# Kernel optimization log

Hardware: AMD Instinct MI355X
Metric: run time of the kernel (lower is better)

Reference implementation:

```python
import jax, jax.numpy as jnp
import numpy as np

N = 6144
INPUT_SIZE = 1024
HIDDEN = 256
NEG_INF = -9e15  # matches torch masked_fill value -9000000000000000.0


def setup_inputs() -> dict:
    key = jax.random.key(0)
    k1, k2, k3, k4 = jax.random.split(key, 4)
    nodes_embed = jax.random.normal(k1, (N, INPUT_SIZE), dtype=jnp.float32)
    node_adj = jax.random.randint(k2, (N, N), 0, 2, dtype=jnp.int32)
    # learned params (xavier-uniform-ish scaling)
    limW = np.sqrt(6.0 / (INPUT_SIZE + HIDDEN))
    W = jax.random.uniform(k3, (INPUT_SIZE, HIDDEN), minval=-limW, maxval=limW, dtype=jnp.float32)
    lima = 1.414 * np.sqrt(6.0 / (2 * HIDDEN + 1))
    a_edge = jax.random.uniform(k4, (2 * HIDDEN,), minval=-lima, maxval=lima, dtype=jnp.float32)
    return {"nodes_embed": nodes_embed, "W": W, "a_edge": a_edge, "node_adj": node_adj}


def reference(nodes_embed, W, a_edge, node_adj):
    # h = nodes_embed @ W : [N, hidden]
    h = nodes_embed @ W
    # W_edge([h_i ; h_j]) decomposes exactly: (h_i @ a1) + (h_j @ a2)
    a1, a2 = a_edge[:HIDDEN], a_edge[HIDDEN:]
    score = (h @ a1)[:, None] + (h @ a2)[None, :]  # [N, N]
    adj_f = node_adj.astype(h.dtype)
    weight = jax.nn.leaky_relu(adj_f * score, negative_slope=0.2)
    weight = jnp.where(node_adj == 0, jnp.asarray(NEG_INF, h.dtype), weight)
    attention = jax.nn.softmax(weight, axis=-1)
    # dropout in eval mode (identity)
    return attention @ h  # [N, hidden]
```

## Files before the change

### kernel.cpp

```cpp
#include <hip/hip_runtime.h>
#include <hip/hip_bf16.h>

#define NN 6144
#define INPUT 1024
#define HID 256

using frag  = __attribute__((ext_vector_type(8))) short;
using f32x4 = __attribute__((ext_vector_type(4))) float;

static __device__ __forceinline__ unsigned short bf16u(float x) {
    unsigned u = __float_as_uint(x);
    u += 0x7fff + ((u >> 16) & 1);
    return (unsigned short)(u >> 16);
}

__global__ __launch_bounds__(256) void k_convert_w(const float* __restrict__ W,
                                                   unsigned short* __restrict__ Wt) {
    int t = blockIdx.x * 256 + threadIdx.x;
    int n = t >> 10, k = t & 1023;
    Wt[t] = bf16u(W[k * HID + n]);
}

__global__ __launch_bounds__(256) void k_gemm1(const float* __restrict__ X,
                                               const unsigned short* __restrict__ Wt,
                                               const float* __restrict__ a_edge,
                                               unsigned short* __restrict__ hT,
                                               float* __restrict__ s1,
                                               float* __restrict__ s2) {
    __shared__ unsigned short A[2][32][72];
    int t = threadIdx.x;
    int m = t >> 3, cg = t & 7;
    int i0 = blockIdx.x * 32, n0 = blockIdx.y * 64;
    int w = t >> 6, l = t & 63, lm = l & 15, q = l >> 4;
    int nw = n0 + w * 16;

    const float* xrow = X + (size_t)(i0 + m) * INPUT + cg * 8;
    const unsigned short* brow = Wt + (size_t)(nw + lm) * INPUT + q * 8;

    f32x4 acc0 = {}, acc1 = {};

    for (int c = 0; c < 16; c++) {
        int buf = c & 1;
        float4 xa = *reinterpret_cast<const float4*>(xrow + c * 64);
        float4 xb = *reinterpret_cast<const float4*>(xrow + c * 64 + 4);
        frag av;
        av[0] = (short)bf16u(xa.x); av[1] = (short)bf16u(xa.y);
        av[2] = (short)bf16u(xa.z); av[3] = (short)bf16u(xa.w);
        av[4] = (short)bf16u(xb.x); av[5] = (short)bf16u(xb.y);
        av[6] = (short)bf16u(xb.z); av[7] = (short)bf16u(xb.w);
        *reinterpret_cast<frag*>(&A[buf][m][cg * 8]) = av;

        __syncthreads();

#pragma unroll
        for (int kk = 0; kk < 2; kk++) {
            frag a0 = *reinterpret_cast<const frag*>(&A[buf][lm][kk * 32 + q * 8]);
            frag a1 = *reinterpret_cast<const frag*>(&A[buf][16 + lm][kk * 32 + q * 8]);
            frag b  = *reinterpret_cast<const frag*>(brow + c * 64 + kk * 32);
            acc0 = __builtin_amdgcn_mfma_f32_16x16x32_bf16(a0, b, acc0, 0, 0, 0);
            acc1 = __builtin_amdgcn_mfma_f32_16x16x32_bf16(a1, b, acc1, 0, 0, 0);
        }
    }

    ushort4 o;
    o.x = bf16u(acc0[0]); o.y = bf16u(acc0[1]); o.z = bf16u(acc0[2]); o.w = bf16u(acc0[3]);
    *reinterpret_cast<ushort4*>(hT + (size_t)(nw + lm) * NN + i0 + q * 4) = o;
    o.x = bf16u(acc1[0]); o.y = bf16u(acc1[1]); o.z = bf16u(acc1[2]); o.w = bf16u(acc1[3]);
    *reinterpret_cast<ushort4*>(hT + (size_t)(nw + lm) * NN + i0 + 16 + q * 4) = o;

    float a1v = a_edge[nw + lm], a2v = a_edge[HID + nw + lm];
#pragma unroll
    for (int h = 0; h < 2; h++) {
        const f32x4& ac = h ? acc1 : acc0;
#pragma unroll
        for (int r = 0; r < 4; r++) {
            float v1 = ac[r] * a1v, v2 = ac[r] * a2v;
            v1 += __shfl_xor(v1, 1); v2 += __shfl_xor(v2, 1);
            v1 += __shfl_xor(v1, 2); v2 += __shfl_xor(v2, 2);
            v1 += __shfl_xor(v1, 4); v2 += __shfl_xor(v2, 4);
            v1 += __shfl_xor(v1, 8); v2 += __shfl_xor(v2, 8);
            if (lm == 0) {
                atomicAdd(&s1[i0 + h * 16 + q * 4 + r], v1);
                atomicAdd(&s2[i0 + h * 16 + q * 4 + r], v2);
            }
        }
    }
}

__global__ __launch_bounds__(256) void k_attn(const int* __restrict__ adj,
                                              const float* __restrict__ s1,
                                              const float* __restrict__ s2,
                                              const unsigned short* __restrict__ hT,
                                              float* __restrict__ U4,
                                              float* __restrict__ denom4) {
    __shared__ unsigned short P[2][32][136];
    int t = threadIdx.x;
    int m = t >> 3, cg = t & 7;
    int i0 = blockIdx.x * 32;
    int q4 = blockIdx.y;
    int j0 = q4 * 1536;
    int w = t >> 6, l = t & 63, lm = l & 15, q = l >> 4;

    float s1v = s1[i0 + m];
    const int*   arow = adj + (size_t)(i0 + m) * NN + j0 + cg * 4;
    const float* s2p  = s2 + j0 + cg * 4;

    const unsigned short* brow[4];
#pragma unroll
    for (int nt = 0; nt < 4; nt++)
        brow[nt] = hT + (size_t)(w * 64 + nt * 16 + lm) * NN + j0 + q * 8;

    f32x4 acc[2][4] = {};
    float dsum = 0.f;

    for (int c = 0; c < 12; c++) {
        int buf = c & 1;
        int jc = c * 128;
#pragma unroll
        for (int p = 0; p < 4; p++) {
            int4   av = *reinterpret_cast<const int4*>(arow + jc + p * 32);
            float4 sv = *reinterpret_cast<const float4*>(s2p + jc + p * 32);
            float sc, wv, p0, p1, p2, p3;
            sc = s1v + sv.x; wv = fmaxf(sc, 0.2f * sc); p0 = av.x ? __expf(wv) : 0.f;
            sc = s1v + sv.y; wv = fmaxf(sc, 0.2f * sc); p1 = av.y ? __expf(wv) : 0.f;
            sc = s1v + sv.z; wv = fmaxf(sc, 0.2f * sc); p2 = av.z ? __expf(wv) : 0.f;
            sc = s1v + sv.w; wv = fmaxf(sc, 0.2f * sc); p3 = av.w ? __expf(wv) : 0.f;
            dsum += (p0 + p1) + (p2 + p3);
            ushort4 pk;
            pk.x = bf16u(p0); pk.y = bf16u(p1); pk.z = bf16u(p2); pk.w = bf16u(p3);
            *reinterpret_cast<ushort4*>(&P[buf][m][p * 32 + cg * 4]) = pk;
        }
        __syncthreads();
#pragma unroll
        for (int kk = 0; kk < 4; kk++) {
            frag a0 = *reinterpret_cast<const frag*>(&P[buf][lm][kk * 32 + q * 8]);
            frag a1 = *reinterpret_cast<const frag*>(&P[buf][16 + lm][kk * 32 + q * 8]);
#pragma unroll
            for (int nt = 0; nt < 4; nt++) {
                frag b = *reinterpret_cast<const frag*>(brow[nt] + jc + kk * 32);
                acc[0][nt] = __builtin_amdgcn_mfma_f32_16x16x32_bf16(a0, b, acc[0][nt], 0, 0, 0);
                acc[1][nt] = __builtin_amdgcn_mfma_f32_16x16x32_bf16(a1, b, acc[1][nt], 0, 0, 0);
            }
        }
    }

    float v = dsum;
    v += __shfl_xor(v, 1); v += __shfl_xor(v, 2); v += __shfl_xor(v, 4);
    if (cg == 0) denom4[(size_t)q4 * NN + i0 + m] = v;

    float* Ub = U4 + (size_t)q4 * NN * HID;
#pragma unroll
    for (int h = 0; h < 2; h++)
#pragma unroll
        for (int nt = 0; nt < 4; nt++)
#pragma unroll
            for (int r = 0; r < 4; r++)
                Ub[(size_t)(i0 + h * 16 + q * 4 + r) * HID + w * 64 + nt * 16 + lm] = acc[h][nt][r];
}

__global__ __launch_bounds__(256) void k_norm(const float* __restrict__ U4,
                                              const float* __restrict__ denom4,
                                              float* __restrict__ out) {
    int i = blockIdx.x, t = threadIdx.x;
    size_t S = (size_t)NN * HID;
    size_t base = (size_t)i * HID + t;
    float u = U4[base] + U4[base + S] + U4[base + 2 * S] + U4[base + 3 * S];
    float d = denom4[i] + denom4[i + NN] + denom4[i + 2 * NN] + denom4[i + 3 * NN];
    out[base] = (d != 0.f) ? u / d : 0.f;
}

extern "C" void kernel_launch(void* const* d_in, const int* in_sizes, int n_in,
                              void* d_out, int out_size, void* d_ws, size_t ws_size,
                              hipStream_t stream) {
    const float* X      = (const float*)d_in[0];
    const float* W      = (const float*)d_in[1];
    const float* a_edge = (const float*)d_in[2];
    const int*   adj    = (const int*)d_in[3];
    float* out = (float*)d_out;

    float* U4     = (float*)d_ws;
    float* denom4 = U4 + (size_t)4 * NN * HID;
    float* s1     = denom4 + (size_t)4 * NN;
    float* s2     = s1 + NN;
    unsigned short* hT = (unsigned short*)(s2 + NN);
    unsigned short* Wt = hT + (size_t)HID * NN;

    hipMemsetAsync(s1, 0, 2 * NN * sizeof(float), stream);
    k_convert_w<<<INPUT * HID / 256, 256, 0, stream>>>(W, Wt);
    k_gemm1<<<dim3(NN / 32, HID / 64), 256, 0, stream>>>(X, Wt, a_edge, hT, s1, s2);
    k_attn<<<dim3(NN / 32, 4), 256, 0, stream>>>(adj, s1, s2, hT, U4, denom4);
    k_norm<<<NN, 256, 0, stream>>>(U4, denom4, out);
}
```

Before: 308.6 us.

## Pre-convert X to bf16, prefetch adjacency, and widen attention blocks to 512 threads

X is now converted to bf16 once in a merged prep kernel, which also transposes W, and stored in the U4 workspace. This stops gemm1 from re-converting the same X rows in each of its four column blocks, and gemm1 now prefetches the next X chunk while computing. The attention kernel goes to 512 threads: each wave owns 32 output columns instead of 64, each thread handles 8 adjacency entries, the next adjacency chunk is loaded one step ahead, and MFMA sections run at raised priority. The aim is more waves to hide latency on the adjacency stream, at the cost of an extra bf16 pass over X in memory and more LDS P-tile reads per output.

```diff
diff --git a/kernel.cpp b/kernel.cpp
--- a/kernel.cpp
+++ b/kernel.cpp
@@ -14,14 +14,29 @@
     return (unsigned short)(u >> 16);
 }
 
-__global__ __launch_bounds__(256) void k_convert_w(const float* __restrict__ W,
-                                                   unsigned short* __restrict__ Wt) {
-    int t = blockIdx.x * 256 + threadIdx.x;
-    int n = t >> 10, k = t & 1023;
-    Wt[t] = bf16u(W[k * HID + n]);
-}
-
-__global__ __launch_bounds__(256) void k_gemm1(const float* __restrict__ X,
+__global__ __launch_bounds__(256) void k_prep(const float* __restrict__ X,
+                                              const float* __restrict__ W,
+                                              unsigned short* __restrict__ Xb,
+                                              unsigned short* __restrict__ Wt) {
+    int b = blockIdx.x;
+    if (b < 3072) {
+        int t = b * 256 + threadIdx.x;
+        const float4* p = reinterpret_cast<const float4*>(X) + (size_t)t * 2;
+        float4 x0 = p[0], x1 = p[1];
+        frag v;
+        v[0] = (short)bf16u(x0.x); v[1] = (short)bf16u(x0.y);
+        v[2] = (short)bf16u(x0.z); v[3] = (short)bf16u(x0.w);
+        v[4] = (short)bf16u(x1.x); v[5] = (short)bf16u(x1.y);
+        v[6] = (short)bf16u(x1.z); v[7] = (short)bf16u(x1.w);
+        *reinterpret_cast<frag*>(Xb + (size_t)t * 8) = v;
+    } else {
+        int t = (b - 3072) * 256 + threadIdx.x;
+        int n = t >> 10, k = t & 1023;
+        Wt[t] = bf16u(W[k * HID + n]);
+    }
+}
+
+__global__ __launch_bounds__(256) void k_gemm1(const unsigned short* __restrict__ Xb,
                                                const unsigned short* __restrict__ Wt,
                                                const float* __restrict__ a_edge,
                                                unsigned short* __restrict__ hT,
@@ -34,22 +49,16 @@
     int w = t >> 6, l = t & 63, lm = l & 15, q = l >> 4;
     int nw = n0 + w * 16;
 
-    const float* xrow = X + (size_t)(i0 + m) * INPUT + cg * 8;
+    const unsigned short* xrow = Xb + (size_t)(i0 + m) * INPUT + cg * 8;
     const unsigned short* brow = Wt + (size_t)(nw + lm) * INPUT + q * 8;
 
     f32x4 acc0 = {}, acc1 = {};
+    frag av = *reinterpret_cast<const frag*>(xrow);
 
     for (int c = 0; c < 16; c++) {
         int buf = c & 1;
-        float4 xa = *reinterpret_cast<const float4*>(xrow + c * 64);
-        float4 xb = *reinterpret_cast<const float4*>(xrow + c * 64 + 4);
-        frag av;
-        av[0] = (short)bf16u(xa.x); av[1] = (short)bf16u(xa.y);
-        av[2] = (short)bf16u(xa.z); av[3] = (short)bf16u(xa.w);
-        av[4] = (short)bf16u(xb.x); av[5] = (short)bf16u(xb.y);
-        av[6] = (short)bf16u(xb.z); av[7] = (short)bf16u(xb.w);
         *reinterpret_cast<frag*>(&A[buf][m][cg * 8]) = av;
-
+        if (c < 15) av = *reinterpret_cast<const frag*>(xrow + (c + 1) * 64);
         __syncthreads();
 
 #pragma unroll
@@ -87,7 +96,7 @@
     }
 }
 
-__global__ __launch_bounds__(256) void k_attn(const int* __restrict__ adj,
+__global__ __launch_bounds__(512) void k_attn(const int* __restrict__ adj,
                                               const float* __restrict__ s1,
                                               const float* __restrict__ s2,
                                               const unsigned short* __restrict__ hT,
@@ -95,67 +104,88 @@
                                               float* __restrict__ denom4) {
     __shared__ unsigned short P[2][32][136];
     int t = threadIdx.x;
-    int m = t >> 3, cg = t & 7;
+    int m = t >> 4, cg = t & 15;
     int i0 = blockIdx.x * 32;
     int q4 = blockIdx.y;
     int j0 = q4 * 1536;
     int w = t >> 6, l = t & 63, lm = l & 15, q = l >> 4;
 
     float s1v = s1[i0 + m];
-    const int*   arow = adj + (size_t)(i0 + m) * NN + j0 + cg * 4;
-    const float* s2p  = s2 + j0 + cg * 4;
-
-    const unsigned short* brow[4];
-#pragma unroll
-    for (int nt = 0; nt < 4; nt++)
-        brow[nt] = hT + (size_t)(w * 64 + nt * 16 + lm) * NN + j0 + q * 8;
-
-    f32x4 acc[2][4] = {};
+    const int*   arow = adj + (size_t)(i0 + m) * NN + j0 + cg * 8;
+    const float* s2p  = s2 + j0 + cg * 8;
+
+    const unsigned short* brow[2];
+#pragma unroll
+    for (int nt = 0; nt < 2; nt++)
+        brow[nt] = hT + (size_t)(w * 32 + nt * 16 + lm) * NN + j0 + q * 8;
+
+    f32x4 acc[2][2] = {};
     float dsum = 0.f;
+
+    int4 ca0 = *reinterpret_cast<const int4*>(arow);
+    int4 ca1 = *reinterpret_cast<const int4*>(arow + 4);
 
     for (int c = 0; c < 12; c++) {
         int buf = c & 1;
         int jc = c * 128;
-#pragma unroll
-        for (int p = 0; p < 4; p++) {
-            int4   av = *reinterpret_cast<const int4*>(arow + jc + p * 32);
-            float4 sv = *reinterpret_cast<const float4*>(s2p + jc + p * 32);
-            float sc, wv, p0, p1, p2, p3;
-            sc = s1v + sv.x; wv = fmaxf(sc, 0.2f * sc); p0 = av.x ? __expf(wv) : 0.f;
-            sc = s1v + sv.y; wv = fmaxf(sc, 0.2f * sc); p1 = av.y ? __expf(wv) : 0.f;
-            sc = s1v + sv.z; wv = fmaxf(sc, 0.2f * sc); p2 = av.z ? __expf(wv) : 0.f;
-            sc = s1v + sv.w; wv = fmaxf(sc, 0.2f * sc); p3 = av.w ? __expf(wv) : 0.f;
-            dsum += (p0 + p1) + (p2 + p3);
-            ushort4 pk;
-            pk.x = bf16u(p0); pk.y = bf16u(p1); pk.z = bf16u(p2); pk.w = bf16u(p3);
-            *reinterpret_cast<ushort4*>(&P[buf][m][p * 32 + cg * 4]) = pk;
-        }
+
+        int4 na0, na1;
+        if (c < 11) {
+            na0 = *reinterpret_cast<const int4*>(arow + jc + 128);
+            na1 = *reinterpret_cast<const int4*>(arow + jc + 132);
+        }
+
+        float4 sv0 = *reinterpret_cast<const float4*>(s2p + jc);
+        float4 sv1 = *reinterpret_cast<const float4*>(s2p + jc + 4);
+        float sc, wv, p0, p1, p2, p3, p4, p5, p6, p7;
+        sc = s1v + sv0.x; wv = fmaxf(sc, 0.2f * sc); p0 = ca0.x ? __expf(wv) : 0.f;
+        sc = s1v + sv0.y; wv = fmaxf(sc, 0.2f * sc); p1 = ca0.y ? __expf(wv) : 0.f;
+        sc = s1v + sv0.z; wv = fmaxf(sc, 0.2f * sc); p2 = ca0.z ? __expf(wv) : 0.f;
+        sc = s1v + sv0.w; wv = fmaxf(sc, 0.2f * sc); p3 = ca0.w ? __expf(wv) : 0.f;
+        sc = s1v + sv1.x; wv = fmaxf(sc, 0.2f * sc); p4 = ca1.x ? __expf(wv) : 0.f;
+        sc = s1v + sv1.y; wv = fmaxf(sc, 0.2f * sc); p5 = ca1.y ? __expf(wv) : 0.f;
+        sc = s1v + sv1.z; wv = fmaxf(sc, 0.2f * sc); p6 = ca1.z ? __expf(wv) : 0.f;
+        sc = s1v + sv1.w; wv = fmaxf(sc, 0.2f * sc); p7 = ca1.w ? __expf(wv) : 0.f;
+        dsum += ((p0 + p1) + (p2 + p3)) + ((p4 + p5) + (p6 + p7));
+        frag pk;
+        pk[0] = (short)bf16u(p0); pk[1] = (short)bf16u(p1);
+        pk[2] = (short)bf16u(p2); pk[3] = (short)bf16u(p3);
+        pk[4] = (short)bf16u(p4); pk[5] = (short)bf16u(p5);
+        pk[6] = (short)bf16u(p6); pk[7] = (short)bf16u(p7);
+        *reinterpret_cast<frag*>(&P[buf][m][cg * 8]) = pk;
+
         __syncthreads();
+
+        __builtin_amdgcn_s_setprio(1);
 #pragma unroll
         for (int kk = 0; kk < 4; kk++) {
             frag a0 = *reinterpret_cast<const frag*>(&P[buf][lm][kk * 32 + q * 8]);
             frag a1 = *reinterpret_cast<const frag*>(&P[buf][16 + lm][kk * 32 + q * 8]);
 #pragma unroll
-            for (int nt = 0; nt < 4; nt++) {
+            for (int nt = 0; nt < 2; nt++) {
                 frag b = *reinterpret_cast<const frag*>(brow[nt] + jc + kk * 32);
                 acc[0][nt] = __builtin_amdgcn_mfma_f32_16x16x32_bf16(a0, b, acc[0][nt], 0, 0, 0);
                 acc[1][nt] = __builtin_amdgcn_mfma_f32_16x16x32_bf16(a1, b, acc[1][nt], 0, 0, 0);
             }
         }
+        __builtin_amdgcn_s_setprio(0);
+
+        ca0 = na0; ca1 = na1;
     }
 
     float v = dsum;
-    v += __shfl_xor(v, 1); v += __shfl_xor(v, 2); v += __shfl_xor(v, 4);
+    v += __shfl_xor(v, 1); v += __shfl_xor(v, 2);
+    v += __shfl_xor(v, 4); v += __shfl_xor(v, 8);
     if (cg == 0) denom4[(size_t)q4 * NN + i0 + m] = v;
 
     float* Ub = U4 + (size_t)q4 * NN * HID;
 #pragma unroll
     for (int h = 0; h < 2; h++)
 #pragma unroll
-        for (int nt = 0; nt < 4; nt++)
+        for (int nt = 0; nt < 2; nt++)
 #pragma unroll
             for (int r = 0; r < 4; r++)
-                Ub[(size_t)(i0 + h * 16 + q * 4 + r) * HID + w * 64 + nt * 16 + lm] = acc[h][nt][r];
+                Ub[(size_t)(i0 + h * 16 + q * 4 + r) * HID + w * 32 + nt * 16 + lm] = acc[h][nt][r];
 }
 
 __global__ __launch_bounds__(256) void k_norm(const float* __restrict__ U4,
@@ -184,10 +214,11 @@
     float* s2     = s1 + NN;
     unsigned short* hT = (unsigned short*)(s2 + NN);
     unsigned short* Wt = hT + (size_t)HID * NN;
+    unsigned short* Xb = (unsigned short*)U4;
 
     hipMemsetAsync(s1, 0, 2 * NN * sizeof(float), stream);
-    k_convert_w<<<INPUT * HID / 256, 256, 0, stream>>>(W, Wt);
-    k_gemm1<<<dim3(NN / 32, HID / 64), 256, 0, stream>>>(X, Wt, a_edge, hT, s1, s2);
-    k_attn<<<dim3(NN / 32, 4), 256, 0, stream>>>(adj, s1, s2, hT, U4, denom4);
+    k_prep<<<3072 + INPUT * HID / 256, 256, 0, stream>>>(X, W, Xb, Wt);
+    k_gemm1<<<dim3(NN / 32, HID / 64), 256, 0, stream>>>(Xb, Wt, a_edge, hT, s1, s2);
+    k_attn<<<dim3(NN / 32, 4), 512, 0, stream>>>(adj, s1, s2, hT, U4, denom4);
     k_norm<<<NN, 256, 0, stream>>>(U4, denom4, out);
 }
```

Result: no change. 310.7 us (+0.7%).
